# Kernel optimization log

Hardware: AMD Instinct MI355X
Metric: run time of the kernel (lower is better)

The kernel has to match this reference:

```python
import jax, jax.numpy as jnp
import numpy as np
from jax import lax

STRIDE = 2  # down_sample_stride
MATMUL_NORM = True


def maxpool2d_5d(x, s):
    # x: [B, T, C, H, W]; kernel=s, stride=s, padding=(s-1)//2 == 0 for s=2
    return lax.reduce_window(
        x, -jnp.inf, lax.max,
        window_dimensions=(1, 1, 1, s, s),
        window_strides=(1, 1, 1, s, s),
        padding='VALID')


def setup_inputs() -> dict:
    key = jax.random.key(0)
    k1, k2, k3, k4 = jax.random.split(key, 4)
    B, T, Ck, Cv, H, W = 2, 4, 64, 256, 64, 64
    return {
        'memory_keys': jax.random.normal(k1, (B, T, Ck, H, W), jnp.float32),
        'memory_values': jax.random.normal(k2, (B, T, Cv, H, W), jnp.float32),
        'query_key': jax.random.normal(k3, (B, Ck, H, W), jnp.float32),
        'query_value': jax.random.normal(k4, (B, Cv, H, W), jnp.float32),
    }


def reference(memory_keys, memory_values, query_key, query_value):
    B, T, Ck, oH, oW = memory_keys.shape
    Cv = memory_values.shape[2]
    # down-sample memory bank (max pool, stride 2, no padding)
    mk = maxpool2d_5d(memory_keys, STRIDE)   # [B,T,Ck,h,w]
    mv = maxpool2d_5d(memory_values, STRIDE) # [B,T,Cv,h,w]
    h, w = mk.shape[-2], mk.shape[-1]
    M = T * h * w
    N = oH * oH  # code uses ori_height*ori_height (square assumed)
    # permute(0,2,1,3,4).view(B,Ck,M).permute(0,2,1) -> [B, M, Ck]
    mk = mk.transpose(0, 2, 1, 3, 4).reshape(B, Ck, M).transpose(0, 2, 1)
    qk = query_key.reshape(B, Ck, N)
    attn = jnp.einsum('bmc,bcn->bmn', mk, qk)  # [B, M, N]
    if MATMUL_NORM:
        attn = attn * (Ck ** -0.5)
    attn = jax.nn.softmax(attn, axis=1)  # softmax over memory positions
    mv = mv.transpose(0, 2, 1, 3, 4).reshape(B, Cv, M)
    memory = jnp.einsum('bcm,bmn->bcn', mv, attn).reshape(B, Cv, oH, oW)
    return jnp.concatenate([query_value, memory], axis=1)  # [B, 2*Cv, H, W]
```

## Files before the change

### kernel.cpp

```cpp
#include <hip/hip_runtime.h>
#include <hip/hip_bf16.h>

typedef unsigned short u16;
typedef unsigned int   u32;
typedef __attribute__((ext_vector_type(8))) short  bf16x8;
typedef __attribute__((ext_vector_type(4))) float  floatx4;

#define NB 2
#define NT 4
#define CK 64
#define CV 256
#define HH 64
#define WW 64
#define MM 4096
#define NN 4096
#define SCALE 0.125f
#define SHIFT 4.0f
#define OUT_B 2097152
#define MSPLIT 2
#define MHALF 2048
#define ITERS 16

__device__ __forceinline__ u16 f2b(float f) {
    __hip_bfloat16 h = __float2bfloat16(f);
    union { __hip_bfloat16 h; u16 u; } v; v.h = h; return v.u;
}


#define KTOT (NB*MM*CK)
__global__ void pool_kv(const float* __restrict__ mk, const float* __restrict__ mv,
                        u16* __restrict__ pk, u16* __restrict__ vt) {
    int e = blockIdx.x * 256 + threadIdx.x;
    if (e < KTOT) {
        int m = e & 4095; int c = (e >> 12) & 63; int b = e >> 18;
        int ww = m & 31, hh = (m >> 5) & 31, t = m >> 10;
        const float* s = mk + ((size_t)(((b*NT + t)*CK + c)*HH + 2*hh))*WW + 2*ww;
        pk[((size_t)b*MM + m)*CK + c] =
            f2b(fmaxf(fmaxf(s[0], s[1]), fmaxf(s[WW], s[WW+1])));
    } else {
        int e2 = e - KTOT;
        int m = e2 & 4095; int c = (e2 >> 12) & 255; int b = e2 >> 20;
        int ww = m & 31, hh = (m >> 5) & 31, t = m >> 10;
        const float* s = mv + ((size_t)(((b*NT + t)*CV + c)*HH + 2*hh))*WW + 2*ww;
        vt[((size_t)b*CV + c)*MM + m] =
            f2b(fmaxf(fmaxf(s[0], s[1]), fmaxf(s[WW], s[WW+1])));
    }
}

__launch_bounds__(512)
__global__ void attn_mfma(const u16* __restrict__ pk, const u16* __restrict__ vt,
                          const float* __restrict__ qk,
                          float* __restrict__ part, float* __restrict__ sums) {
    const int ntile = blockIdx.x, b = blockIdx.y, ms = blockIdx.z;
    const int tid = threadIdx.x, w = tid >> 6, l = tid & 63;
    const int lrow = l & 15, quad = l >> 4;
    const int n0 = ntile * 64;
    const int m0 = ms * MHALF;

    __shared__ u16  P[64 * 128];
    __shared__ float sums_s[8][64];

    bf16x8 qf[2][4];
    const float* qb = qk + (size_t)b * CK * NN;
    #pragma unroll
    for (int cc = 0; cc < 2; ++cc)
        #pragma unroll
        for (int t = 0; t < 4; ++t) {
            int n = n0 + t*16 + lrow;
            #pragma unroll
            for (int i = 0; i < 8; ++i) {
                int c = cc*32 + quad*8 + i;
                qf[cc][t][i] = (short)f2b(qb[(size_t)c*NN + n]);
            }
        }

    const u16* pkb = pk + (size_t)b * MM * CK;
    const u16* vtb = vt + (size_t)b * CV * MM;

    floatx4 oacc[2][4];
    #pragma unroll
    for (int j = 0; j < 2; ++j)
        #pragma unroll
        for (int t = 0; t < 4; ++t)
            oacc[j][t] = (floatx4){0.f, 0.f, 0.f, 0.f};
    float sacc[4] = {0.f, 0.f, 0.f, 0.f};

    const int sw = lrow << 1;

    for (int it = 0; it < ITERS; ++it) {
        const int mbase = m0 + it * 128;

        const u16* kp = pkb + (size_t)(mbase + w*16 + lrow)*CK + quad*8;
        bf16x8 kf0 = *(const bf16x8*)(kp);
        bf16x8 kf1 = *(const bf16x8*)(kp + 32);

        bf16x8 vf[4][2];
        #pragma unroll
        for (int j = 0; j < 2; ++j) {
            const u16* vp = vtb + (size_t)(w*32 + j*16 + lrow)*MM + mbase + quad*8;
            vf[0][j] = *(const bf16x8*)(vp);
            vf[1][j] = *(const bf16x8*)(vp + 32);
            vf[2][j] = *(const bf16x8*)(vp + 64);
            vf[3][j] = *(const bf16x8*)(vp + 96);
        }

        #pragma unroll
        for (int t = 0; t < 4; ++t) {
            floatx4 s = __builtin_amdgcn_mfma_f32_16x16x32_bf16(
                            kf0, qf[0][t], (floatx4){0.f,0.f,0.f,0.f}, 0, 0, 0);
            s = __builtin_amdgcn_mfma_f32_16x16x32_bf16(kf1, qf[1][t], s, 0, 0, 0);
            float p0 = __expf(s[0]*SCALE - SHIFT);
            float p1 = __expf(s[1]*SCALE - SHIFT);
            float p2 = __expf(s[2]*SCALE - SHIFT);
            float p3 = __expf(s[3]*SCALE - SHIFT);
            sacc[t] += (p0 + p1) + (p2 + p3);
            u32 d0 = (u32)f2b(p0) | ((u32)f2b(p1) << 16);
            u32 d1 = (u32)f2b(p2) | ((u32)f2b(p3) << 16);
            int n_l = t*16 + lrow;
            int cb  = (w << 2) + quad;
            *(uint2*)&P[n_l*128 + ((cb ^ sw) << 2)] = make_uint2(d0, d1);
        }
        __syncthreads();

        #pragma unroll
        for (int cc = 0; cc < 4; ++cc) {
            bf16x8 pf[4];
            #pragma unroll
            for (int t = 0; t < 4; ++t) {
                int n_l = t*16 + lrow;
                int cb  = (cc << 3) + (quad << 1);
                pf[t] = *(const bf16x8*)&P[n_l*128 + ((cb ^ sw) << 2)];
            }
            #pragma unroll
            for (int j = 0; j < 2; ++j)
                #pragma unroll
                for (int t = 0; t < 4; ++t)
                    oacc[j][t] = __builtin_amdgcn_mfma_f32_16x16x32_bf16(
                                     vf[cc][j], pf[t], oacc[j][t], 0, 0, 0);
        }
        __syncthreads();
    }

    #pragma unroll
    for (int t = 0; t < 4; ++t) {
        float v = sacc[t];
        v += __shfl_xor(v, 16, 64);
        v += __shfl_xor(v, 32, 64);
        if (l < 16) sums_s[w][t*16 + l] = v;
    }
    __syncthreads();

    float* pb = part + ((size_t)((ms*NB + b)*64 + ntile)) * (256*64);
    #pragma unroll
    for (int j = 0; j < 2; ++j)
        #pragma unroll
        for (int t = 0; t < 4; ++t)
            #pragma unroll
            for (int r = 0; r < 4; ++r) {
                int c = w*32 + j*16 + quad*4 + r;
                int n = t*16 + lrow;
                pb[c*64 + n] = oacc[j][t][r];
            }
    if (tid < 64) {
        float sv = 0.f;
        #pragma unroll
        for (int ww2 = 0; ww2 < 8; ++ww2) sv += sums_s[ww2][tid];
        sums[((size_t)((ms*NB + b)*64 + ntile))*64 + tid] = sv;
    }
}

__global__ void epilogue(const float* __restrict__ part, const float* __restrict__ sums,
                         const float4* __restrict__ qv, float* __restrict__ out) {
    int e = blockIdx.x * 256 + threadIdx.x;
    if (e < 524288) {
        int b = e >> 18; int ru = e & 262143;
        ((float4*)out)[(size_t)b*(OUT_B/4) + ru] = qv[e];
    } else {
        int e4 = e - 524288;
        int nl4   = e4 & 15;
        int ntile = (e4 >> 4) & 63;
        int c     = (e4 >> 10) & 255;
        int b     = e4 >> 18;
        size_t t0 = (size_t)(0*NB + b)*64 + ntile;
        size_t t1 = (size_t)(1*NB + b)*64 + ntile;
        const float4* p4 = (const float4*)part;
        const float4* s4 = (const float4*)sums;
        float4 u0 = p4[t0*4096 + c*16 + nl4];
        float4 u1 = p4[t1*4096 + c*16 + nl4];
        float4 d0 = s4[t0*16 + nl4];
        float4 d1 = s4[t1*16 + nl4];
        float4 r;
        r.x = (u0.x + u1.x) / (d0.x + d1.x);
        r.y = (u0.y + u1.y) / (d0.y + d1.y);
        r.z = (u0.z + u1.z) / (d0.z + d1.z);
        r.w = (u0.w + u1.w) / (d0.w + d1.w);
        ((float4*)out)[(size_t)(b*512 + 256 + c)*1024 + ntile*16 + nl4] = r;
    }
}


__global__ void pool_v_f32(const float* __restrict__ src, float* __restrict__ out) {
    int e = blockIdx.x * 256 + threadIdx.x;
    int c = e & 255;
    int r = e >> 8;
    int ww = r & 31;  int hh = (r >> 5) & 31;
    int t  = (r >> 10) & 3;  int b = r >> 12;
    int m  = r & (MM - 1);
    const float* s = src + ((size_t)(((b*NT + t)*CV + c)*HH + 2*hh))*WW + 2*ww;
    out[(size_t)b*OUT_B + (size_t)m*CV + c] = fmaxf(fmaxf(s[0], s[1]), fmaxf(s[WW], s[WW+1]));
}

__global__ void pool_k_f32(const float* __restrict__ src, float* __restrict__ dst) {
    int e = blockIdx.x * 256 + threadIdx.x;
    int c = e & 63;
    int r = e >> 6;
    int ww = r & 31;  int hh = (r >> 5) & 31;
    int t  = (r >> 10) & 3;  int b = r >> 12;
    const float* s = src + ((size_t)(((b*NT + t)*CK + c)*HH + 2*hh))*WW + 2*ww;
    dst[e] = fmaxf(fmaxf(s[0], s[1]), fmaxf(s[WW], s[WW+1]));
}

__global__ void copy_qv_f32(const float4* __restrict__ src, float4* __restrict__ dst) {
    int u = blockIdx.x * 256 + threadIdx.x;
    int b  = u >> 18;
    int ru = u & 262143;
    dst[(size_t)b * (OUT_B/4) + ru] = src[u];
}

template<bool STAGED_K>
__launch_bounds__(256)
__global__ void attn_old(const float* __restrict__ pk,
                         const float* __restrict__ mk,
                         const float* __restrict__ qk,
                         float* __restrict__ out) {
    __shared__ __align__(16) float q_lds[CK][4];
    __shared__ __align__(16) float sarr[4][MM];
    __shared__ float inv_l[4];

    const int tid = threadIdx.x;
    const int blk = blockIdx.x;
    const int b   = blk >> 10;
    const int n0  = (blk & 1023) << 2;

    {
        int c = tid >> 2, qi = tid & 3;
        q_lds[c][qi] = qk[((size_t)(b*CK + c))*NN + n0 + qi];
    }
    __syncthreads();

    #pragma unroll
    for (int i = 0; i < 16; ++i) {
        int m = tid + (i << 8);
        float a0 = 0.f, a1 = 0.f, a2 = 0.f, a3 = 0.f;
        if (STAGED_K) {
            const float4* k4 = reinterpret_cast<const float4*>(pk + ((size_t)b*MM + m)*CK);
            #pragma unroll
            for (int cc = 0; cc < 16; ++cc) {
                float4 kv = k4[cc];
                int c = cc*4;
                float4 q0 = *reinterpret_cast<const float4*>(&q_lds[c][0]);
                float4 q1 = *reinterpret_cast<const float4*>(&q_lds[c+1][0]);
                float4 q2 = *reinterpret_cast<const float4*>(&q_lds[c+2][0]);
                float4 q3 = *reinterpret_cast<const float4*>(&q_lds[c+3][0]);
                a0 += kv.x*q0.x + kv.y*q1.x + kv.z*q2.x + kv.w*q3.x;
                a1 += kv.x*q0.y + kv.y*q1.y + kv.z*q2.y + kv.w*q3.y;
                a2 += kv.x*q0.z + kv.y*q1.z + kv.z*q2.z + kv.w*q3.z;
                a3 += kv.x*q0.w + kv.y*q1.w + kv.z*q2.w + kv.w*q3.w;
            }
        } else {
            int ww = m & 31, hh = (m >> 5) & 31, t = m >> 10;
            const float* base = mk + ((size_t)((b*NT + t)*CK)*HH + 2*hh)*WW + 2*ww;
            for (int c = 0; c < CK; ++c) {
                const float* s = base + (size_t)c*HH*WW;
                float kv = fmaxf(fmaxf(s[0], s[1]), fmaxf(s[WW], s[WW+1]));
                float4 q = *reinterpret_cast<const float4*>(&q_lds[c][0]);
                a0 += kv*q.x; a1 += kv*q.y; a2 += kv*q.z; a3 += kv*q.w;
            }
        }
        sarr[0][m] = a0*SCALE;
        sarr[1][m] = a1*SCALE;
        sarr[2][m] = a2*SCALE;
        sarr[3][m] = a3*SCALE;
    }
    __syncthreads();

    const int wave = tid >> 6, lane = tid & 63;
    float mx = -3.0e38f;
    for (int m = lane; m < MM; m += 64) mx = fmaxf(mx, sarr[wave][m]);
    #pragma unroll
    for (int off = 32; off > 0; off >>= 1) mx = fmaxf(mx, __shfl_xor(mx, off, 64));
    float ls = 0.f;
    for (int m = lane; m < MM; m += 64) {
        float p = __expf(sarr[wave][m] - mx);
        sarr[wave][m] = p;
        ls += p;
    }
    #pragma unroll
    for (int off = 32; off > 0; off >>= 1) ls += __shfl_xor(ls, off, 64);
    if (lane == 0) inv_l[wave] = 1.0f / ls;
    __syncthreads();

    const int c4 = lane;
    const float4* vb = reinterpret_cast<const float4*>(out + (size_t)b*OUT_B) + c4;
    const float* prow = sarr[wave];
    float a0 = 0.f, a1 = 0.f, a2 = 0.f, a3 = 0.f;
    for (int m = 0; m < MM; m += 4) {
        float4 p4 = *reinterpret_cast<const float4*>(prow + m);
        const float4* vp = vb + (size_t)m*(CV/4);
        float4 v0 = vp[0], v1 = vp[CV/4], v2 = vp[CV/2], v3 = vp[3*(CV/4)];
        a0 += p4.x*v0.x + p4.y*v1.x + p4.z*v2.x + p4.w*v3.x;
        a1 += p4.x*v0.y + p4.y*v1.y + p4.z*v2.y + p4.w*v3.y;
        a2 += p4.x*v0.z + p4.y*v1.z + p4.z*v2.z + p4.w*v3.z;
        a3 += p4.x*v0.w + p4.y*v1.w + p4.z*v2.w + p4.w*v3.w;
    }

    float inv = inv_l[wave];
    int n = n0 + wave;
    size_t ob = ((size_t)(b*512 + 256 + c4*4))*NN + n;
    out[ob]        = a0*inv;
    out[ob + NN]   = a1*inv;
    out[ob + 2*NN] = a2*inv;
    out[ob + 3*NN] = a3*inv;
}


extern "C" void kernel_launch(void* const* d_in, const int* in_sizes, int n_in,
                              void* d_out, int out_size, void* d_ws, size_t ws_size,
                              hipStream_t stream) {
    const float* mk = (const float*)d_in[0];
    const float* mv = (const float*)d_in[1];
    const float* qk = (const float*)d_in[2];
    const float* qv = (const float*)d_in[3];
    float* out = (float*)d_out;

    u16* pk_bf = (u16*)d_ws;
    u16* vt_bf = pk_bf + (size_t)NB*MM*CK;
    float* part = (float*)(vt_bf + (size_t)NB*CV*MM);
    float* sums = part + 4194304;
    const size_t need = (size_t)NB*MM*CK*2 + (size_t)NB*CV*MM*2
                      + (4194304 + 16384) * sizeof(float);

    if (ws_size >= need) {
        pool_kv<<<(KTOT + NB*MM*CV)/256, 256, 0, stream>>>(mk, mv, pk_bf, vt_bf);
        attn_mfma<<<dim3(64, NB, MSPLIT), 512, 0, stream>>>(pk_bf, vt_bf, qk, part, sums);
        epilogue<<<(2*524288)/256, 256, 0, stream>>>(part, sums, (const float4*)qv, out);
    } else {
        const size_t pk_bytes = (size_t)NB*MM*CK*sizeof(float);
        const bool staged = (ws_size >= pk_bytes);
        float* pk = (float*)d_ws;
        pool_v_f32<<<(NB*MM*CV)/256, 256, 0, stream>>>(mv, out);
        if (staged) {
            pool_k_f32<<<(NB*MM*CK)/256, 256, 0, stream>>>(mk, pk);
            attn_old<true ><<<NB*(NN/4), 256, 0, stream>>>(pk, mk, qk, out);
        } else {
            attn_old<false><<<NB*(NN/4), 256, 0, stream>>>(pk, mk, qk, out);
        }
        copy_qv_f32<<<((NB*CV*HH*WW)/4)/256, 256, 0, stream>>>((const float4*)qv, (float4*)out);
    }
}
```

Measured before the change: 148.2 us.

## Split attention over four M-chunks, double-buffer P, vectorize pooling, move qv copy

```diff
diff --git a/kernel.cpp b/kernel.cpp
--- a/kernel.cpp
+++ b/kernel.cpp
@@ -17,9 +17,6 @@
 #define SCALE 0.125f
 #define SHIFT 4.0f
 #define OUT_B 2097152
-#define MSPLIT 2
-#define MHALF 2048
-#define ITERS 16
 
 __device__ __forceinline__ u16 f2b(float f) {
     __hip_bfloat16 h = __float2bfloat16(f);
@@ -27,37 +24,61 @@
 }
 
 
-#define KTOT (NB*MM*CK)
+#define KP 262144
+#define VP 1048576
+#define QTOT4 524288
 __global__ void pool_kv(const float* __restrict__ mk, const float* __restrict__ mv,
-                        u16* __restrict__ pk, u16* __restrict__ vt) {
+                        const float4* __restrict__ qv,
+                        u16* __restrict__ pk, u16* __restrict__ vt,
+                        float* __restrict__ out) {
     int e = blockIdx.x * 256 + threadIdx.x;
-    if (e < KTOT) {
-        int m = e & 4095; int c = (e >> 12) & 63; int b = e >> 18;
-        int ww = m & 31, hh = (m >> 5) & 31, t = m >> 10;
-        const float* s = mk + ((size_t)(((b*NT + t)*CK + c)*HH + 2*hh))*WW + 2*ww;
-        pk[((size_t)b*MM + m)*CK + c] =
-            f2b(fmaxf(fmaxf(s[0], s[1]), fmaxf(s[WW], s[WW+1])));
+    if (e < KP) {
+        int q  = e & 15;
+        int hh = (e >> 4) & 31;
+        int t  = (e >> 9) & 3;
+        int c  = (e >> 11) & 63;
+        int b  = e >> 17;
+        const float4* s = (const float4*)mk
+                        + ((size_t)(((b*NT + t)*CK + c)*HH + 2*hh))*16 + q;
+        float4 r0 = s[0], r1 = s[16];
+        int m = t*1024 + hh*32 + 2*q;
+        u16* d = pk + ((size_t)b*MM + m)*CK + c;
+        d[0]  = f2b(fmaxf(fmaxf(r0.x, r0.y), fmaxf(r1.x, r1.y)));
+        d[CK] = f2b(fmaxf(fmaxf(r0.z, r0.w), fmaxf(r1.z, r1.w)));
+    } else if (e < KP + VP) {
+        int e2 = e - KP;
+        int q  = e2 & 15;
+        int hh = (e2 >> 4) & 31;
+        int t  = (e2 >> 9) & 3;
+        int c  = (e2 >> 11) & 255;
+        int b  = e2 >> 19;
+        const float4* s = (const float4*)mv
+                        + ((size_t)(((b*NT + t)*CV + c)*HH + 2*hh))*16 + q;
+        float4 r0 = s[0], r1 = s[16];
+        int m = t*1024 + hh*32 + 2*q;
+        u32 lo = f2b(fmaxf(fmaxf(r0.x, r0.y), fmaxf(r1.x, r1.y)));
+        u32 hi = f2b(fmaxf(fmaxf(r0.z, r0.w), fmaxf(r1.z, r1.w)));
+        *(u32*)&vt[((size_t)b*CV + c)*MM + m] = lo | (hi << 16);
     } else {
-        int e2 = e - KTOT;
-        int m = e2 & 4095; int c = (e2 >> 12) & 255; int b = e2 >> 20;
-        int ww = m & 31, hh = (m >> 5) & 31, t = m >> 10;
-        const float* s = mv + ((size_t)(((b*NT + t)*CV + c)*HH + 2*hh))*WW + 2*ww;
-        vt[((size_t)b*CV + c)*MM + m] =
-            f2b(fmaxf(fmaxf(s[0], s[1]), fmaxf(s[WW], s[WW+1])));
-    }
-}
-
-__launch_bounds__(512)
+        int e3 = e - (KP + VP);
+        int b = e3 >> 18; int ru = e3 & 262143;
+        ((float4*)out)[(size_t)b*(OUT_B/4) + ru] = qv[e3];
+    }
+}
+
+template<int ITERS>
+__launch_bounds__(512, 4)
 __global__ void attn_mfma(const u16* __restrict__ pk, const u16* __restrict__ vt,
                           const float* __restrict__ qk,
                           float* __restrict__ part, float* __restrict__ sums) {
-    const int ntile = blockIdx.x, b = blockIdx.y, ms = blockIdx.z;
+    const int ntile = blockIdx.y;
+    const int b  = blockIdx.x & 1, ms = blockIdx.x >> 1;
     const int tid = threadIdx.x, w = tid >> 6, l = tid & 63;
     const int lrow = l & 15, quad = l >> 4;
     const int n0 = ntile * 64;
-    const int m0 = ms * MHALF;
-
-    __shared__ u16  P[64 * 128];
+    const int m0 = ms * (ITERS * 128);
+
+    __shared__ u16  P[2][64 * 128];
     __shared__ float sums_s[8][64];
 
     bf16x8 qf[2][4];
@@ -89,6 +110,7 @@
 
     for (int it = 0; it < ITERS; ++it) {
         const int mbase = m0 + it * 128;
+        u16* Pb = &P[it & 1][0];
 
         const u16* kp = pkb + (size_t)(mbase + w*16 + lrow)*CK + quad*8;
         bf16x8 kf0 = *(const bf16x8*)(kp);
@@ -118,7 +140,7 @@
             u32 d1 = (u32)f2b(p2) | ((u32)f2b(p3) << 16);
             int n_l = t*16 + lrow;
             int cb  = (w << 2) + quad;
-            *(uint2*)&P[n_l*128 + ((cb ^ sw) << 2)] = make_uint2(d0, d1);
+            *(uint2*)&Pb[n_l*128 + ((cb ^ sw) << 2)] = make_uint2(d0, d1);
         }
         __syncthreads();
 
@@ -128,8 +150,8 @@
             #pragma unroll
             for (int t = 0; t < 4; ++t) {
                 int n_l = t*16 + lrow;
-                int cb  = (cc << 3) + (quad << 1);
-                pf[t] = *(const bf16x8*)&P[n_l*128 + ((cb ^ sw) << 2)];
+                int ch  = (cc << 3) + (quad << 1);
+                pf[t] = *(const bf16x8*)&Pb[n_l*128 + ((ch ^ sw) << 2)];
             }
             #pragma unroll
             for (int j = 0; j < 2; ++j)
@@ -138,7 +160,6 @@
                     oacc[j][t] = __builtin_amdgcn_mfma_f32_16x16x32_bf16(
                                      vf[cc][j], pf[t], oacc[j][t], 0, 0, 0);
         }
-        __syncthreads();
     }
 
     #pragma unroll
@@ -169,33 +190,28 @@
     }
 }
 
+template<int MS>
 __global__ void epilogue(const float* __restrict__ part, const float* __restrict__ sums,
-                         const float4* __restrict__ qv, float* __restrict__ out) {
+                         float* __restrict__ out) {
     int e = blockIdx.x * 256 + threadIdx.x;
-    if (e < 524288) {
-        int b = e >> 18; int ru = e & 262143;
-        ((float4*)out)[(size_t)b*(OUT_B/4) + ru] = qv[e];
-    } else {
-        int e4 = e - 524288;
-        int nl4   = e4 & 15;
-        int ntile = (e4 >> 4) & 63;
-        int c     = (e4 >> 10) & 255;
-        int b     = e4 >> 18;
-        size_t t0 = (size_t)(0*NB + b)*64 + ntile;
-        size_t t1 = (size_t)(1*NB + b)*64 + ntile;
-        const float4* p4 = (const float4*)part;
-        const float4* s4 = (const float4*)sums;
-        float4 u0 = p4[t0*4096 + c*16 + nl4];
-        float4 u1 = p4[t1*4096 + c*16 + nl4];
-        float4 d0 = s4[t0*16 + nl4];
-        float4 d1 = s4[t1*16 + nl4];
-        float4 r;
-        r.x = (u0.x + u1.x) / (d0.x + d1.x);
-        r.y = (u0.y + u1.y) / (d0.y + d1.y);
-        r.z = (u0.z + u1.z) / (d0.z + d1.z);
-        r.w = (u0.w + u1.w) / (d0.w + d1.w);
-        ((float4*)out)[(size_t)(b*512 + 256 + c)*1024 + ntile*16 + nl4] = r;
-    }
+    int nl4   = e & 15;
+    int ntile = (e >> 4) & 63;
+    int c     = (e >> 10) & 255;
+    int b     = (e >> 18) & 1;
+    const float4* p4 = (const float4*)part;
+    const float4* s4 = (const float4*)sums;
+    float4 num = {0.f,0.f,0.f,0.f}, den = {0.f,0.f,0.f,0.f};
+    #pragma unroll
+    for (int ms = 0; ms < MS; ++ms) {
+        size_t ts = (size_t)(ms*NB + b)*64 + ntile;
+        float4 u = p4[ts*4096 + c*16 + nl4];
+        float4 d = s4[ts*16 + nl4];
+        num.x += u.x; num.y += u.y; num.z += u.z; num.w += u.w;
+        den.x += d.x; den.y += d.y; den.z += d.z; den.w += d.w;
+    }
+    float4 r;
+    r.x = num.x/den.x; r.y = num.y/den.y; r.z = num.z/den.z; r.w = num.w/den.w;
+    ((float4*)out)[(size_t)(b*512 + 256 + c)*1024 + ntile*16 + nl4] = r;
 }
 
 
@@ -336,24 +352,34 @@
     u16* pk_bf = (u16*)d_ws;
     u16* vt_bf = pk_bf + (size_t)NB*MM*CK;
     float* part = (float*)(vt_bf + (size_t)NB*CV*MM);
-    float* sums = part + 4194304;
-    const size_t need = (size_t)NB*MM*CK*2 + (size_t)NB*CV*MM*2
-                      + (4194304 + 16384) * sizeof(float);
-
-    if (ws_size >= need) {
-        pool_kv<<<(KTOT + NB*MM*CV)/256, 256, 0, stream>>>(mk, mv, pk_bf, vt_bf);
-        attn_mfma<<<dim3(64, NB, MSPLIT), 512, 0, stream>>>(pk_bf, vt_bf, qk, part, sums);
-        epilogue<<<(2*524288)/256, 256, 0, stream>>>(part, sums, (const float4*)qv, out);
+
+    const size_t base   = (size_t)NB*MM*CK*2 + (size_t)NB*CV*MM*2;
+    const size_t need_A = base + (8388608 + 32768) * sizeof(float);
+    const size_t need_B = base + (4194304 + 16384) * sizeof(float);
+    const int pool_blocks = (KP + VP + QTOT4) / 256;
+
+    if (ws_size >= need_A) {
+        float* sums = part + 8388608;
+        pool_kv<<<pool_blocks, 256, 0, stream>>>(mk, mv, (const float4*)qv,
+                                                 pk_bf, vt_bf, out);
+        attn_mfma<8><<<dim3(8, 64), 512, 0, stream>>>(pk_bf, vt_bf, qk, part, sums);
+        epilogue<4><<<524288/256, 256, 0, stream>>>(part, sums, out);
+    } else if (ws_size >= need_B) {
+        float* sums = part + 4194304;
+        pool_kv<<<pool_blocks, 256, 0, stream>>>(mk, mv, (const float4*)qv,
+                                                 pk_bf, vt_bf, out);
+        attn_mfma<16><<<dim3(4, 64), 512, 0, stream>>>(pk_bf, vt_bf, qk, part, sums);
+        epilogue<2><<<524288/256, 256, 0, stream>>>(part, sums, out);
     } else {
         const size_t pk_bytes = (size_t)NB*MM*CK*sizeof(float);
         const bool staged = (ws_size >= pk_bytes);
-        float* pk = (float*)d_ws;
+        float* pkf = (float*)d_ws;
         pool_v_f32<<<(NB*MM*CV)/256, 256, 0, stream>>>(mv, out);
         if (staged) {
-            pool_k_f32<<<(NB*MM*CK)/256, 256, 0, stream>>>(mk, pk);
-            attn_old<true ><<<NB*(NN/4), 256, 0, stream>>>(pk, mk, qk, out);
+            pool_k_f32<<<(NB*MM*CK)/256, 256, 0, stream>>>(mk, pkf);
+            attn_old<true ><<<NB*(NN/4), 256, 0, stream>>>(pkf, mk, qk, out);
         } else {
-            attn_old<false><<<NB*(NN/4), 256, 0, stream>>>(pk, mk, qk, out);
+            attn_old<false><<<NB*(NN/4), 256, 0, stream>>>(pkf, mk, qk, out);
         }
         copy_qv_f32<<<((NB*CV*HH*WW)/4)/256, 256, 0, stream>>>((const float4*)qv, (float4*)out);
     }
```

After: 161.0 us. 1.09x slower.
